# Kernel tuning notes

Hardware: AMD Instinct MI355X
Metric: run time of the kernel (lower is better)

Reference implementation:

```python
import jax, jax.numpy as jnp
import numpy as np

D = 1024      # model dim
H = 16        # num heads
HD = D // H   # head dim = 64
B, N, M = 4, 4096, 256
EPS = 1e-12   # torch F.normalize eps


def setup_inputs() -> dict:
    key = jax.random.key(0)
    ks = jax.random.split(key, 11)
    s = 0.02  # weight init scale
    W = lambda k: jax.random.normal(k, (D, D), jnp.float32) * s
    return {
        "x": jax.random.normal(ks[0], (B, N, D), jnp.float32),
        "c": jax.random.normal(ks[1], (B, M, D), jnp.float32),
        "Wq_x": W(ks[2]), "Wk_x": W(ks[3]), "Wv_x": W(ks[4]),
        "Wq_c": W(ks[5]), "Wk_c": W(ks[6]), "Wv_c": W(ks[7]),
        "Wo_x": W(ks[8]), "Wo_c": W(ks[9]),
        "norm_const": 0.5 * jnp.ones((1, H, 1, 1), jnp.float32),
    }


def _heads(t):
    # (B, S, D) -> (B, H, S, HD)
    b, s, _ = t.shape
    return t.reshape(b, s, H, HD).transpose(0, 2, 1, 3)


def _l2norm(t):
    n = jnp.linalg.norm(t, axis=-1, keepdims=True)
    return t / jnp.maximum(n, EPS)


def reference(x, c, Wq_x, Wk_x, Wv_x, Wq_c, Wk_c, Wv_c, Wo_x, Wo_c, norm_const):
    b, n, d = x.shape
    m = c.shape[1]
    # fused QKV projections for each stream (Linear, no bias: y = t @ W^T)
    qx = _l2norm(_heads(x @ Wq_x.T))   # (B,H,N,HD), cosine-normalized
    kx = _l2norm(_heads(x @ Wk_x.T))
    vx = _heads(x @ Wv_x.T)
    qc = _l2norm(_heads(c @ Wq_c.T))   # (B,H,M,HD)
    kc = _l2norm(_heads(c @ Wk_c.T))
    vc = _heads(c @ Wv_c.T)
    # concat streams along the sequence axis
    q = jnp.concatenate([qx, qc], axis=2)   # (B,H,N+M,HD)
    k = jnp.concatenate([kx, kc], axis=2)
    v = jnp.concatenate([vx, vc], axis=2)
    n_tot = n + m
    # cosine (linear) attention, non-causal: values scaled by N^sigmoid(norm_const)
    v = v / (jnp.float32(n_tot) ** jax.nn.sigmoid(norm_const))
    kv = jnp.einsum("bhnd,bhne->bhde", k, v)         # (B,H,HD,HD)
    attn = jnp.einsum("bhnd,bhde->bhne", q, kv)      # (B,H,N+M,HD)
    # split streams, merge heads, output projections
    attn_x = attn[:, :, :n].transpose(0, 2, 1, 3).reshape(b, n, H * HD)
    attn_c = attn[:, :, n:].transpose(0, 2, 1, 3).reshape(b, m, H * HD)
    out_x = attn_x @ Wo_x.T
    out_c = attn_c @ Wo_c.T
    return out_x, out_c
```

## Files before the change

kernel.cpp:

```cpp
#include <hip/hip_runtime.h>
#include <cstdint>

typedef unsigned int u32;
typedef unsigned short u16;
typedef float fx4 __attribute__((ext_vector_type(4)));
typedef __bf16 bfx8 __attribute__((ext_vector_type(8)));

__device__ __forceinline__ u16 f2bf(float f) {
  u32 u = __builtin_bit_cast(u32, f);
  u32 r = (u + 0x7fffu + ((u >> 16) & 1u)) >> 16;
  return (u16)r;
}
__device__ __forceinline__ float bf2f(u16 v) {
  return __builtin_bit_cast(float, (u32)v << 16);
}
__device__ __forceinline__ void async_copy16(const void* g, void* l) {
  auto gp = reinterpret_cast<__attribute__((address_space(1))) void*>((uintptr_t)g);
  auto lp = reinterpret_cast<__attribute__((address_space(3))) void*>((uintptr_t)l);
  __builtin_amdgcn_global_load_lds(gp, lp, 16, 0, 0);
}

__global__ __launch_bounds__(256) void cvt_all(
    const float* __restrict__ x, const float* __restrict__ c,
    const float* __restrict__ w0, const float* __restrict__ w1,
    const float* __restrict__ w2, const float* __restrict__ w3,
    const float* __restrict__ w4, const float* __restrict__ w5,
    const float* __restrict__ w6, const float* __restrict__ w7,
    u16* __restrict__ xb, u16* __restrict__ cb, u16* __restrict__ wb) {
  const int i = blockIdx.x * 256 + threadIdx.x;
  const float* src;
  u16* dst;
  size_t off;
  if (i < 4194304) {
    src = x; dst = xb; off = (size_t)i;
  } else if (i < 4456448) {
    src = c; dst = cb; off = (size_t)(i - 4194304);
  } else {
    const int r = i - 4456448;
    const int wsel = r >> 18;
    off = (size_t)(r & 262143);
    switch (wsel) {
      case 0: src = w0; break; case 1: src = w1; break;
      case 2: src = w2; break; case 3: src = w3; break;
      case 4: src = w4; break; case 5: src = w5; break;
      case 6: src = w6; break; default: src = w7; break;
    }
    dst = wb + (size_t)wsel * 1048576;
  }
  const fx4 v = *(const fx4*)(src + off * 4);
  uint2 o;
  o.x = (u32)f2bf(v[0]) | ((u32)f2bf(v[1]) << 16);
  o.y = (u32)f2bf(v[2]) | ((u32)f2bf(v[3]) << 16);
  *(uint2*)(dst + off * 4) = o;
}

#define GC_DSB(BUF, KS)                                                        \
  _Pragma("unroll") for (int i_ = 0; i_ < 4; ++i_) bfr[i_] =                   \
      *(const bfx8*)(lds + (BUF) + 16384 + (KS) * 8192 + wc * 2048 + i_ * 512 + aLane);
#define GC_DSA(BUF, KS, H)                                                     \
  _Pragma("unroll") for (int i_ = 0; i_ < 4; ++i_) af[i_] =                    \
      *(const bfx8*)(lds + (BUF) + (KS) * 8192 + wr * 4096 + (H) * 2048 + i_ * 512 + aLane);
#define GC_STA(REG, KCOL)                                                      \
  async_copy16(Aop + aOff0 + (KCOL), lds + (REG) + dst0);                      \
  async_copy16(Aop + aOff1 + (KCOL), lds + (REG) + dst1);
#define GC_STB(REG, KCOL)                                                      \
  async_copy16(Bop + bOff0 + (KCOL), lds + (REG) + dst0);                      \
  async_copy16(Bop + bOff1 + (KCOL), lds + (REG) + dst1);
#define GC_MFMA(H)                                                             \
  __builtin_amdgcn_s_setprio(1);                                               \
  _Pragma("unroll") for (int mi_ = 0; mi_ < 4; ++mi_)                          \
  _Pragma("unroll") for (int ni_ = 0; ni_ < 4; ++ni_)                          \
      acc[(H) * 4 + mi_][ni_] = __builtin_amdgcn_mfma_f32_16x16x32_bf16(       \
          af[mi_], bfr[ni_], acc[(H) * 4 + mi_][ni_], 0, 0, 0);                \
  __builtin_amdgcn_s_setprio(0);
#define GC_MID()                                                               \
  __builtin_amdgcn_s_barrier();                                                \
  asm volatile("s_waitcnt lgkmcnt(0)" ::: "memory");                           \
  __builtin_amdgcn_sched_barrier(0);
#define GC_END()                                                               \
  __builtin_amdgcn_s_barrier();                                                \
  __builtin_amdgcn_sched_barrier(0);

__device__ __forceinline__ void gemm256_core(
    const u16* __restrict__ Aop, const u16* __restrict__ Bop,
    long rowBase, long colBase, u16* lds, fx4 (&acc)[8][4]) {
  const int t = threadIdx.x;
  const int lane = t & 63;
  const int lr = lane & 15;
  const int quad = lane >> 4;
  const int w = t >> 6;
  const int wr = w >> 2;
  const int wc = w & 3;
  const int phys = (((lr & 1) << 2) | quad) ^ ((lr >> 1) & 7);
  const int aLane = ((lr >> 1) << 6) + (phys << 3);

  int aOff0, aOff1, bOff0, bOff1, dst0, dst1;
  {
    const int c0 = t;
    const int R0 = c0 >> 3;
    const int lg0 = (c0 & 7) ^ (R0 & 7);
    const int m0_ = 2 * R0 + (lg0 >> 2);
    const int g0 = lg0 & 3;
    aOff0 = (int)(rowBase + m0_) * 1024 + g0 * 8;
    bOff0 = (int)(colBase + m0_) * 1024 + g0 * 8;
    dst0 = c0 * 8;
    const int c1 = t + 512;
    const int R1 = c1 >> 3;
    const int lg1 = (c1 & 7) ^ (R1 & 7);
    const int m1_ = 2 * R1 + (lg1 >> 2);
    const int g1 = lg1 & 3;
    aOff1 = (int)(rowBase + m1_) * 1024 + g1 * 8;
    bOff1 = (int)(colBase + m1_) * 1024 + g1 * 8;
    dst1 = c1 * 8;
  }

  GC_STA(0, 0) GC_STB(16384, 0) GC_STA(8192, 32) GC_STB(24576, 32)
  GC_STA(32768, 64) GC_STB(49152, 64)
  asm volatile("s_waitcnt vmcnt(8)" ::: "memory");
  __builtin_amdgcn_s_barrier();
  __builtin_amdgcn_sched_barrier(0);

  bfx8 bfr[4];
  for (int it = 0; it < 8; ++it) {
    const bool firstI = (it == 0);
    const bool lastI = (it == 7);
    const int k1 = (2 * it + 1) * 64 + 32;
    const int k2 = (2 * it + 2) * 64;
    const int k3 = k2 + 32;
    const int k4 = (2 * it + 3) * 64;
    { bfx8 af[4];
      GC_DSB(0, 0) GC_DSA(0, 0, 0)
      GC_STA(40960, k1)
      GC_MID() GC_MFMA(0) GC_END() }
    { bfx8 af[4];
      GC_DSA(0, 0, 1)
      GC_STB(57344, k1)
      GC_MID() GC_MFMA(1)
      if (firstI) { asm volatile("s_waitcnt vmcnt(8)" ::: "memory"); }
      GC_END() }
    { bfx8 af[4];
      GC_DSB(0, 1) GC_DSA(0, 1, 0)
      if (!lastI) { GC_STA(0, k2) }
      GC_MID() GC_MFMA(0) GC_END() }
    { bfx8 af[4];
      GC_DSA(0, 1, 1)
      if (!lastI) { GC_STB(16384, k2) }
      GC_MID() GC_MFMA(1)
      if (firstI) { asm volatile("s_waitcnt vmcnt(8)" ::: "memory"); }
      else        { asm volatile("s_waitcnt vmcnt(4)" ::: "memory"); }
      GC_END() }
    { bfx8 af[4];
      GC_DSB(32768, 0) GC_DSA(32768, 0, 0)
      if (!lastI) { GC_STA(8192, k3) }
      GC_MID() GC_MFMA(0) GC_END() }
    { bfx8 af[4];
      GC_DSA(32768, 0, 1)
      if (!lastI) { GC_STB(24576, k3) }
      GC_MID() GC_MFMA(1)
      if (firstI)     { asm volatile("s_waitcnt vmcnt(8)" ::: "memory"); }
      else if (lastI) { asm volatile("s_waitcnt vmcnt(0)" ::: "memory"); }
      GC_END() }
    { bfx8 af[4];
      GC_DSB(32768, 1) GC_DSA(32768, 1, 0)
      if (!lastI) { GC_STA(32768, k4) }
      GC_MID() GC_MFMA(0) GC_END() }
    { bfx8 af[4];
      GC_DSA(32768, 1, 1)
      if (!lastI) { GC_STB(49152, k4) }
      GC_MID() GC_MFMA(1)
      if (firstI)      { asm volatile("s_waitcnt vmcnt(8)" ::: "memory"); }
      else if (!lastI) { asm volatile("s_waitcnt vmcnt(4)" ::: "memory"); }
      GC_END() }
  }
}

__global__ __launch_bounds__(512, 2) void proj_fused(
    const u16* __restrict__ Xb, const u16* __restrict__ Cb, const u16* __restrict__ Wb,
    u16* __restrict__ Qx, u16* __restrict__ Qc,
    u16* __restrict__ Kt, u16* __restrict__ Vt,
    const float* __restrict__ nc) {
  extern __shared__ __align__(16) u16 lds[];
  const int bid = (int)(blockIdx.y * 12 + blockIdx.x);
  const int u = (bid & 7) * 102 + (bid >> 3);
  const int yy = u / 12;
  const int xx = u - yy * 12;
  const bool isC = yy >= 64;
  const u16* A = isC ? Cb : Xb;
  const u16* Bw = Wb + (isC ? 3145728 : 0);
  const long rowBase = (long)(isC ? yy - 64 : yy) * 256;
  const long colBase = (long)xx * 256;

  fx4 acc[8][4] = {};
  gemm256_core(A, Bw, rowBase, colBase, lds, acc);

  const int t = threadIdx.x;
  const int lane = t & 63;
  const int lr = lane & 15;
  const int quad = lane >> 4;
  const int w = t >> 6;
  const int wr = w >> 2;
  const int wc = w & 3;
  const long wRowBase = rowBase + wr * 128;

  const long col0 = colBase + wc * 64;
  const int col64 = (int)(col0 >> 6);
  const int sel = col64 >> 4;
  const int h = col64 & 15;
  const int lcolBase = (int)(col0 & 1023);

  if (sel == 0) {
    u16* dst = isC ? Qc : Qx;
#pragma unroll
    for (int mi = 0; mi < 8; ++mi) {
      float ss[4] = {0.f, 0.f, 0.f, 0.f};
#pragma unroll
      for (int ni = 0; ni < 4; ++ni)
#pragma unroll
        for (int r = 0; r < 4; ++r) ss[r] += acc[mi][ni][r] * acc[mi][ni][r];
#pragma unroll
      for (int off = 1; off < 16; off <<= 1)
#pragma unroll
        for (int r = 0; r < 4; ++r) ss[r] += __shfl_xor(ss[r], off, 64);
      float sc[4];
#pragma unroll
      for (int r = 0; r < 4; ++r) sc[r] = 1.f / fmaxf(sqrtf(ss[r]), 1e-12f);
#pragma unroll
      for (int ni = 0; ni < 4; ++ni) {
        const long col = lcolBase + ni * 16 + lr;
#pragma unroll
        for (int r = 0; r < 4; ++r) {
          const long row = wRowBase + mi * 16 + quad * 4 + r;
          dst[row * 1024 + col] = f2bf(acc[mi][ni][r] * sc[r]);
        }
      }
    }
  } else {
    __syncthreads();
    u16* LT = lds + w * 8192;
    u16* T = (sel == 1) ? Kt : Vt;
    int b, nglob0;
    if (!isC) { b = (int)(wRowBase >> 12); nglob0 = (int)(wRowBase & 4095); }
    else      { b = (int)(wRowBase >> 8);  nglob0 = 4096 + (int)(wRowBase & 255); }
    u16* Tw = T + (size_t)(b * 16 + h) * 64 * 4352;
    const float vs = __expf(-8.3783908f / (1.f + __expf(-nc[h])));

#pragma unroll
    for (int mi = 0; mi < 8; ++mi) {
      float sc[4];
      if (sel == 1) {
        float ss[4] = {0.f, 0.f, 0.f, 0.f};
#pragma unroll
        for (int ni = 0; ni < 4; ++ni)
#pragma unroll
          for (int r = 0; r < 4; ++r) ss[r] += acc[mi][ni][r] * acc[mi][ni][r];
#pragma unroll
        for (int off = 1; off < 16; off <<= 1)
#pragma unroll
          for (int r = 0; r < 4; ++r) ss[r] += __shfl_xor(ss[r], off, 64);
#pragma unroll
        for (int r = 0; r < 4; ++r) sc[r] = 1.f / fmaxf(sqrtf(ss[r]), 1e-12f);
      } else {
#pragma unroll
        for (int r = 0; r < 4; ++r) sc[r] = vs;
      }
      const int g = mi * 2 + (quad >> 1);
      const int sub = (quad & 1) * 4;
#pragma unroll
      for (int ni = 0; ni < 4; ++ni) {
        const int d = ni * 16 + lr;
        uint2 o;
        o.x = (u32)f2bf(acc[mi][ni][0] * sc[0]) | ((u32)f2bf(acc[mi][ni][1] * sc[1]) << 16);
        o.y = (u32)f2bf(acc[mi][ni][2] * sc[2]) | ((u32)f2bf(acc[mi][ni][3] * sc[3]) << 16);
        *(uint2*)&LT[d * 128 + ((g ^ (d & 15)) << 3) + sub] = o;
      }
    }
    __syncthreads();
    const int d = lane;
    u16* drow = Tw + (size_t)d * 4352 + nglob0;
#pragma unroll
    for (int j = 0; j < 16; ++j) {
      const uint4 qv = *(const uint4*)&LT[d * 128 + ((j ^ (d & 15)) << 3)];
      *(uint4*)&drow[j * 8] = qv;
    }
  }
}

__global__ __launch_bounds__(256) void kv_mfma(
    const u16* __restrict__ Kt, const u16* __restrict__ Vt, float* __restrict__ kvp) {
  __shared__ __align__(16) u16 TT[4][2][4096];
  const int bh = blockIdx.x;
  const int t = threadIdx.x;
  const int w = t >> 6;
  const int lane = t & 63;
  const int lr = lane & 15;
  const int quad = lane >> 4;
  const u16* Ksrc = Kt + (size_t)bh * 64 * 4352;
  const u16* Vsrc = Vt + (size_t)bh * 64 * 4352;
  const int row8 = lane >> 3;
  const int gst = lane & 7;
  fx4 acc[4][4] = {};

  const int kbase = (blockIdx.y * 4 + w) * 64;
#pragma unroll
  for (int i = 0; i < 8; ++i) {
    const int row = i * 8 + row8;
    const int col = ((gst ^ (row & 7)) << 3);
    const size_t go = (size_t)row * 4352 + kbase + col;
    async_copy16(Ksrc + go, &TT[w][0][i * 512 + lane * 8]);
    async_copy16(Vsrc + go, &TT[w][1][i * 512 + lane * 8]);
  }
  __syncthreads();
#pragma unroll
  for (int ks = 0; ks < 2; ++ks) {
    bfx8 af[4], bfr[4];
    const int g = ((ks * 4 + quad) ^ (lr & 7)) << 3;
#pragma unroll
    for (int i = 0; i < 4; ++i) af[i] = *(const bfx8*)&TT[w][0][(i * 16 + lr) * 64 + g];
#pragma unroll
    for (int i = 0; i < 4; ++i) bfr[i] = *(const bfx8*)&TT[w][1][(i * 16 + lr) * 64 + g];
#pragma unroll
    for (int mi = 0; mi < 4; ++mi)
#pragma unroll
      for (int ni = 0; ni < 4; ++ni)
        acc[mi][ni] =
            __builtin_amdgcn_mfma_f32_16x16x32_bf16(af[mi], bfr[ni], acc[mi][ni], 0, 0, 0);
  }
  __syncthreads();
  float* red = (float*)&TT[0][0][0];
  float* my = red + w * 4096;
#pragma unroll
  for (int mi = 0; mi < 4; ++mi)
#pragma unroll
    for (int ni = 0; ni < 4; ++ni) {
      const int e = ni * 16 + lr;
      const int dg = mi * 4 + quad;
      *(fx4*)&my[e * 64 + ((dg ^ (e & 15)) << 2)] = acc[mi][ni];
    }
  __syncthreads();
  float* outp = kvp + ((size_t)blockIdx.y * 64 + bh) * 4096;
#pragma unroll
  for (int j = 0; j < 4; ++j) {
    const int L = t * 16 + j * 4;
    const int e = L >> 6;
    const int dg = (L >> 2) & 15;
    const int addr = e * 64 + ((dg ^ (e & 15)) << 2);
    fx4 sv = *(const fx4*)&red[addr];
    sv += *(const fx4*)&red[4096 + addr];
    sv += *(const fx4*)&red[8192 + addr];
    sv += *(const fx4*)&red[12288 + addr];
    *(fx4*)&outp[L] = sv;
  }
}

__global__ __launch_bounds__(256) void kv_reduce(
    const float* __restrict__ kvp, float* __restrict__ kvb) {
  const int o = blockIdx.x * 256 + threadIdx.x;
  const int bh = o >> 10;
  const int idx = (o & 1023) * 4;
  fx4 s = {0.f, 0.f, 0.f, 0.f};
#pragma unroll
  for (int y = 0; y < 17; ++y)
    s += *(const fx4*)&kvp[((size_t)y * 64 + bh) * 4096 + idx];
  *(fx4*)&kvb[(size_t)bh * 4096 + idx] = s;
}

__global__ __launch_bounds__(256) void weff_build(
    const u16* __restrict__ WoX, const u16* __restrict__ WoC,
    const float* __restrict__ kvb, u16* __restrict__ WeffX, u16* __restrict__ WeffC) {
  const int ot = blockIdx.x;
  const int bh = blockIdx.y;
  const int b = bh >> 4, h = bh & 15;
  const u16* Wo = blockIdx.z ? WoC : WoX;
  u16* outp = (blockIdx.z ? WeffC : WeffX) + (size_t)b * 1048576;

  __shared__ __align__(16) float kvT[64 * 64];
  __shared__ __align__(16) float WoT[64 * 64];
  const int t = threadIdx.x;
#pragma unroll
  for (int j = 0; j < 4; ++j) {
    const int idx = (t + 256 * j) * 4;
    *(fx4*)&kvT[idx] = *(const fx4*)&kvb[(size_t)bh * 4096 + idx];
  }
#pragma unroll
  for (int j = 0; j < 2; ++j) {
    const int u = t + 256 * j;
    const int row = u >> 3;
    const int e0 = (u & 7) * 8;
    const uint4 q = *(const uint4*)&Wo[(size_t)(ot * 64 + row) * 1024 + h * 64 + e0];
    WoT[(e0 + 0) * 64 + row] = bf2f((u16)(q.x & 0xffff));
    WoT[(e0 + 1) * 64 + row] = bf2f((u16)(q.x >> 16));
    WoT[(e0 + 2) * 64 + row] = bf2f((u16)(q.y & 0xffff));
    WoT[(e0 + 3) * 64 + row] = bf2f((u16)(q.y >> 16));
    WoT[(e0 + 4) * 64 + row] = bf2f((u16)(q.z & 0xffff));
    WoT[(e0 + 5) * 64 + row] = bf2f((u16)(q.z >> 16));
    WoT[(e0 + 6) * 64 + row] = bf2f((u16)(q.w & 0xffff));
    WoT[(e0 + 7) * 64 + row] = bf2f((u16)(q.w >> 16));
  }
  __syncthreads();
  const int ob = (t >> 4) * 4;
  const int db = (t & 15) * 4;
  float acc[4][4] = {};
#pragma unroll 4
  for (int e = 0; e < 64; ++e) {
    const fx4 wv = *(const fx4*)&WoT[e * 64 + ob];
    const fx4 kvv = *(const fx4*)&kvT[e * 64 + db];
#pragma unroll
    for (int i = 0; i < 4; ++i)
#pragma unroll
      for (int j = 0; j < 4; ++j)
        acc[i][j] += wv[i] * kvv[j];
  }
#pragma unroll
  for (int i = 0; i < 4; ++i)
#pragma unroll
    for (int j = 0; j < 4; ++j)
      outp[(size_t)(ot * 64 + ob + i) * 1024 + h * 64 + db + j] = f2bf(acc[i][j]);
}

__global__ __launch_bounds__(512, 2) void out_fused(
    const u16* __restrict__ Qx, const u16* __restrict__ Qc,
    const u16* __restrict__ Wex, const u16* __restrict__ Wec,
    float* __restrict__ out) {
  extern __shared__ __align__(16) u16 lds[];
  const int bid = (int)(blockIdx.y * 4 + blockIdx.x);
  const int u = (bid & 7) * 34 + (bid >> 3);
  const int yt = u >> 2;
  const int xx = u & 3;
  const int b = yt / 17;
  const int l = yt - b * 17;
  const bool isC = (l == 16);
  const u16* A;
  const u16* Bw;
  float* C;
  long rowBase;
  if (!isC) {
    A = Qx + (size_t)b * 4194304;
    Bw = Wex + (size_t)b * 1048576;
    C = out + (size_t)b * 4194304;
    rowBase = (long)l * 256;
  } else {
    A = Qc + (size_t)b * 262144;
    Bw = Wec + (size_t)b * 1048576;
    C = out + 16777216 + (size_t)b * 262144;
    rowBase = 0;
  }
  const long colBase = (long)xx * 256;

  fx4 acc[8][4] = {};
  gemm256_core(A, Bw, rowBase, colBase, lds, acc);

  const int t = threadIdx.x;
  const int lane = t & 63;
  const int lr = lane & 15;
  const int quad = lane >> 4;
  const int w = t >> 6;
  const int wr = w >> 2;
  const int wc = w & 3;
#pragma unroll
  for (int mi = 0; mi < 8; ++mi)
#pragma unroll
    for (int ni = 0; ni < 4; ++ni) {
      const long col = colBase + wc * 64 + ni * 16 + lr;
#pragma unroll
      for (int r = 0; r < 4; ++r) {
        const long row = rowBase + wr * 128 + mi * 16 + quad * 4 + r;
        C[row * 1024 + col] = acc[mi][ni][r];
      }
    }
}

extern "C" void kernel_launch(void* const* d_in, const int* in_sizes, int n_in,
                              void* d_out, int out_size, void* d_ws, size_t ws_size,
                              hipStream_t stream) {
  (void)in_sizes; (void)n_in; (void)out_size; (void)ws_size;
  const float* x = (const float*)d_in[0];
  const float* c = (const float*)d_in[1];
  const float* nc = (const float*)d_in[10];
  float* out = (float*)d_out;
  char* ws = (char*)d_ws;

  static bool attr_done = false;
  if (!attr_done) {
    hipFuncSetAttribute((const void*)proj_fused,
                        hipFuncAttributeMaxDynamicSharedMemorySize, 131072);
    hipFuncSetAttribute((const void*)out_fused,
                        hipFuncAttributeMaxDynamicSharedMemorySize, 131072);
    attr_done = true;
  }

  u16* Xb = (u16*)(ws + 0);
  u16* Cb = (u16*)(ws + 33554432);
  u16* Wb = (u16*)(ws + 35651584);
  u16* Qx = (u16*)(ws + 52428800);
  u16* Qc = (u16*)(ws + 85983232);
  u16* Kt = (u16*)(ws + 88080384);
  u16* Vt = (u16*)(ws + 123731968);
  float* kvb = (float*)(ws + 159383552);
  u16* Weffx = (u16*)(ws + 160432128);
  u16* Weffc = (u16*)(ws + 168820736);
  float* kvp = (float*)(ws + 0);

  cvt_all<<<25600, 256, 0, stream>>>(
      x, c, (const float*)d_in[2], (const float*)d_in[3], (const float*)d_in[4],
      (const float*)d_in[5], (const float*)d_in[6], (const float*)d_in[7],
      (const float*)d_in[8], (const float*)d_in[9], Xb, Cb, Wb);

  proj_fused<<<dim3(12, 68), 512, 131072, stream>>>(Xb, Cb, Wb, Qx, Qc, Kt, Vt, nc);
  kv_mfma<<<dim3(64, 17), 256, 0, stream>>>(Kt, Vt, kvp);
  kv_reduce<<<256, 256, 0, stream>>>(kvp, kvb);
  weff_build<<<dim3(16, 64, 2), 256, 0, stream>>>(Wb + 6 * 1048576, Wb + 7 * 1048576,
                                                  kvb, Weffx, Weffc);
  out_fused<<<dim3(4, 68), 512, 131072, stream>>>(Qx, Qc, Weffx, Weffc, out);
}
```

Before: 392.1 us.

## Use 128x256 output tiles in out_fused GEMM to double block count

Adds a gemm128_core that computes 128-row by 256-column tiles with double-buffered async LDS loads, and switches the output-projection kernel to it, launching 544 blocks instead of 272. LDS per block drops to 96KB. The intent is better CU occupancy and load balance on the final GEMM, since 272 large tiles fill the 256 CUs unevenly. The cost is less operand reuse per tile, so B-operand traffic per output element roughly doubles.

```diff
diff --git a/kernel.cpp b/kernel.cpp
--- a/kernel.cpp
+++ b/kernel.cpp
@@ -285,6 +285,92 @@
   }
 }
 
+__device__ __forceinline__ void gemm128_core(
+    const u16* __restrict__ Aop, const u16* __restrict__ Bop,
+    long rowBase, long colBase, u16* lds, fx4 (&acc)[4][4]) {
+  const int t = threadIdx.x;
+  const int lane = t & 63;
+  const int lr = lane & 15;
+  const int quad = lane >> 4;
+  const int w = t >> 6;
+  const int wr = w >> 2;
+  const int wc = w & 3;
+  const int phys = (((lr & 1) << 2) | quad) ^ ((lr >> 1) & 7);
+  const int aLane = ((lr >> 1) << 6) + (phys << 3);
+
+  int aOffA, bOffB0, bOffB1, dstA, dstB0, dstB1;
+  {
+    const int c0 = t;
+    const int RA = c0 >> 3;
+    const int lgA = (c0 & 7) ^ (RA & 7);
+    aOffA = (int)(rowBase + 2 * RA + (lgA >> 2)) * 1024 + (lgA & 3) * 8;
+    dstA = c0 * 8;
+    const int RB0 = c0 >> 3;
+    const int lgB0 = (c0 & 7) ^ (RB0 & 7);
+    bOffB0 = (int)(colBase + 2 * RB0 + (lgB0 >> 2)) * 1024 + (lgB0 & 3) * 8;
+    dstB0 = c0 * 8;
+    const int c1 = t + 512;
+    const int RB1 = c1 >> 3;
+    const int lgB1 = (c1 & 7) ^ (RB1 & 7);
+    bOffB1 = (int)(colBase + 2 * RB1 + (lgB1 >> 2)) * 1024 + (lgB1 & 3) * 8;
+    dstB1 = c1 * 8;
+  }
+
+#define O_ST(QB, KT, KS)                                                       \
+  async_copy16(Aop + aOffA + (KT) * 64 + (KS) * 32, lds + (QB) + (KS) * 4096 + dstA); \
+  async_copy16(Bop + bOffB0 + (KT) * 64 + (KS) * 32, lds + (QB) + 8192 + (KS) * 8192 + dstB0); \
+  async_copy16(Bop + bOffB1 + (KT) * 64 + (KS) * 32, lds + (QB) + 8192 + (KS) * 8192 + dstB1);
+#define O_DS(QB, KS)                                                           \
+  _Pragma("unroll") for (int i_ = 0; i_ < 4; ++i_) af[i_] =                    \
+      *(const bfx8*)(lds + (QB) + (KS) * 4096 + wr * 2048 + i_ * 512 + aLane); \
+  _Pragma("unroll") for (int i_ = 0; i_ < 4; ++i_) bfr[i_] =                   \
+      *(const bfx8*)(lds + (QB) + 8192 + (KS) * 8192 + wc * 2048 + i_ * 512 + aLane);
+#define O_MFMA()                                                               \
+  __builtin_amdgcn_s_setprio(1);                                               \
+  _Pragma("unroll") for (int mi_ = 0; mi_ < 4; ++mi_)                          \
+  _Pragma("unroll") for (int ni_ = 0; ni_ < 4; ++ni_)                          \
+      acc[mi_][ni_] = __builtin_amdgcn_mfma_f32_16x16x32_bf16(                 \
+          af[mi_], bfr[ni_], acc[mi_][ni_], 0, 0, 0);                          \
+  __builtin_amdgcn_s_setprio(0);
+
+  O_ST(0, 0, 0) O_ST(0, 0, 1)
+  asm volatile("s_waitcnt vmcnt(3)" ::: "memory");
+  __builtin_amdgcn_s_barrier();
+  __builtin_amdgcn_sched_barrier(0);
+
+  for (int kt = 0; kt < 16; ++kt) {
+    const int qb = (kt & 1) * 24576;
+    const int nq = ((kt + 1) & 1) * 24576;
+    const bool lastK = (kt == 15);
+    { bfx8 af[4], bfr[4];
+      O_DS(qb, 0)
+      if (!lastK) { O_ST(nq, kt + 1, 0) }
+      __builtin_amdgcn_s_barrier();
+      asm volatile("s_waitcnt lgkmcnt(0)" ::: "memory");
+      __builtin_amdgcn_sched_barrier(0);
+      O_MFMA()
+      __builtin_amdgcn_sched_barrier(0);
+      if (lastK) { asm volatile("s_waitcnt vmcnt(0)" ::: "memory"); }
+      else       { asm volatile("s_waitcnt vmcnt(3)" ::: "memory"); }
+      __builtin_amdgcn_s_barrier();
+      __builtin_amdgcn_sched_barrier(0); }
+    { bfx8 af[4], bfr[4];
+      O_DS(qb, 1)
+      if (!lastK) { O_ST(nq, kt + 1, 1) }
+      __builtin_amdgcn_s_barrier();
+      asm volatile("s_waitcnt lgkmcnt(0)" ::: "memory");
+      __builtin_amdgcn_sched_barrier(0);
+      O_MFMA()
+      __builtin_amdgcn_sched_barrier(0);
+      if (!lastK) { asm volatile("s_waitcnt vmcnt(3)" ::: "memory"); }
+      __builtin_amdgcn_s_barrier();
+      __builtin_amdgcn_sched_barrier(0); }
+  }
+#undef O_ST
+#undef O_DS
+#undef O_MFMA
+}
+
 __global__ __launch_bounds__(256) void kv_mfma(
     const u16* __restrict__ Kt, const u16* __restrict__ Vt, float* __restrict__ kvp) {
   __shared__ __align__(16) u16 TT[4][2][4096];
@@ -423,12 +509,12 @@
     float* __restrict__ out) {
   extern __shared__ __align__(16) u16 lds[];
   const int bid = (int)(blockIdx.y * 4 + blockIdx.x);
-  const int u = (bid & 7) * 34 + (bid >> 3);
+  const int u = (bid & 7) * 68 + (bid >> 3);
   const int yt = u >> 2;
   const int xx = u & 3;
-  const int b = yt / 17;
-  const int l = yt - b * 17;
-  const bool isC = (l == 16);
+  const int b = yt / 34;
+  const int l = yt - b * 34;
+  const bool isC = (l >= 32);
   const u16* A;
   const u16* Bw;
   float* C;
@@ -437,17 +523,17 @@
     A = Qx + (size_t)b * 4194304;
     Bw = Wex + (size_t)b * 1048576;
     C = out + (size_t)b * 4194304;
-    rowBase = (long)l * 256;
+    rowBase = (long)l * 128;
   } else {
     A = Qc + (size_t)b * 262144;
     Bw = Wec + (size_t)b * 1048576;
     C = out + 16777216 + (size_t)b * 262144;
-    rowBase = 0;
+    rowBase = (long)(l - 32) * 128;
   }
   const long colBase = (long)xx * 256;
 
-  fx4 acc[8][4] = {};
-  gemm256_core(A, Bw, rowBase, colBase, lds, acc);
+  fx4 acc[4][4] = {};
+  gemm128_core(A, Bw, rowBase, colBase, lds, acc);
 
   const int t = threadIdx.x;
   const int lane = t & 63;
@@ -457,13 +543,13 @@
   const int wr = w >> 2;
   const int wc = w & 3;
 #pragma unroll
-  for (int mi = 0; mi < 8; ++mi)
+  for (int mi = 0; mi < 4; ++mi)
 #pragma unroll
     for (int ni = 0; ni < 4; ++ni) {
       const long col = colBase + wc * 64 + ni * 16 + lr;
 #pragma unroll
       for (int r = 0; r < 4; ++r) {
-        const long row = rowBase + wr * 128 + mi * 16 + quad * 4 + r;
+        const long row = rowBase + wr * 64 + mi * 16 + quad * 4 + r;
         C[row * 1024 + col] = acc[mi][ni][r];
       }
     }
@@ -484,7 +570,7 @@
     hipFuncSetAttribute((const void*)proj_fused,
                         hipFuncAttributeMaxDynamicSharedMemorySize, 131072);
     hipFuncSetAttribute((const void*)out_fused,
-                        hipFuncAttributeMaxDynamicSharedMemorySize, 131072);
+                        hipFuncAttributeMaxDynamicSharedMemorySize, 98304);
     attr_done = true;
   }
 
@@ -510,5 +596,5 @@
   kv_reduce<<<256, 256, 0, stream>>>(kvp, kvb);
   weff_build<<<dim3(16, 64, 2), 256, 0, stream>>>(Wb + 6 * 1048576, Wb + 7 * 1048576,
                                                   kvb, Weffx, Weffc);
-  out_fused<<<dim3(4, 68), 512, 131072, stream>>>(Qx, Qc, Weffx, Weffc, out);
-}
+  out_fused<<<dim3(4, 136), 512, 98304, stream>>>(Qx, Qc, Weffx, Weffc, out);
+}
```

New measurement: 387.3 us. No clear change (-1.2%).
